# Kernel tuning notes

Hardware: AMD Instinct MI355X
Metric: run time of the kernel (lower is better)

Reference implementation:

```python
import jax, jax.numpy as jnp
import numpy as np

C = 256
NH = 8
G = 32  # groupnorm groups (min(32, C))
EPS = 1e-6


def setup_inputs() -> dict:
    key = jax.random.key(0)
    ks = jax.random.split(key, 7)
    B, D, H, W = 2, 16, 16, 16
    x = jax.random.normal(ks[0], (B, C, D, H, W), dtype=jnp.float32)
    gn_gamma = jnp.ones((C,), jnp.float32)
    gn_beta = jnp.zeros((C,), jnp.float32)
    s = 1.0 / np.sqrt(C)
    qkv_w = jax.random.normal(ks[1], (3 * C, C), jnp.float32) * s  # 1x1x1 conv weight
    qkv_b = jnp.zeros((3 * C,), jnp.float32)
    proj_w = jax.random.normal(ks[2], (C, C), jnp.float32) * s
    proj_b = jnp.zeros((C,), jnp.float32)
    return {"x": x, "gn_gamma": gn_gamma, "gn_beta": gn_beta,
            "qkv_w": qkv_w, "qkv_b": qkv_b, "proj_w": proj_w, "proj_b": proj_b}


def _group_norm(x, gamma, beta):
    # x: [B, C, S]
    B, Cc, S = x.shape
    xg = x.reshape(B, G, (Cc // G) * S)
    mu = xg.mean(axis=-1, keepdims=True)
    var = xg.var(axis=-1, keepdims=True)
    xg = (xg - mu) * jax.lax.rsqrt(var + EPS)
    x = xg.reshape(B, Cc, S)
    return x * gamma[None, :, None] + beta[None, :, None]


def reference(x, gn_gamma, gn_beta, qkv_w, qkv_b, proj_w, proj_b):
    B, Cc, D, H, W = x.shape
    S = D * H * W
    hd = Cc // NH
    xf = x.reshape(B, Cc, S)
    h = _group_norm(xf, gn_gamma, gn_beta)
    # 1x1x1 conv == channel matmul: [B, 3C, S]
    qkv = jnp.einsum('oc,bcs->bos', qkv_w, h) + qkv_b[None, :, None]
    # torch path: reshape(B,3C,S).permute(0,2,1).chunk -> q=channels[0:C]
    q, k, v = qkv[:, :Cc], qkv[:, Cc:2 * Cc], qkv[:, 2 * Cc:]
    # [B, C, S] -> [B, NH, S, hd]
    def to_heads(t):
        return t.reshape(B, NH, hd, S).transpose(0, 1, 3, 2)
    q, k, v = to_heads(q), to_heads(k), to_heads(v)
    scale = hd ** (-0.5)
    attn = jax.nn.softmax(jnp.einsum('bnqd,bnkd->bnqk', q, k) * scale, axis=-1)
    o = jnp.einsum('bnqk,bnkd->bnqd', attn, v)  # [B, NH, S, hd]
    o = o.transpose(0, 1, 3, 2).reshape(B, Cc, S)  # back to [B, C, S]
    o = jnp.einsum('oc,bcs->bos', proj_w, o) + proj_b[None, :, None]
    return x + o.reshape(B, Cc, D, H, W)
```

## Files before the change

kernel.cpp:

```cpp
#include <hip/hip_runtime.h>
#include <cstddef>

#define S_LEN 4096
#define C_DIM 256
#define NHEADS 8
#define HDIM 32

typedef __attribute__((ext_vector_type(8))) _Float16 half8;
typedef __attribute__((ext_vector_type(4))) _Float16 half4;
typedef __attribute__((ext_vector_type(2))) _Float16 h2t;
typedef __attribute__((ext_vector_type(2))) __fp16 fp16x2;
typedef __attribute__((ext_vector_type(4))) float floatx4;

#define SC2F ((float)(0.17677669529663687 * 1.4426950408889634))

__global__ __launch_bounds__(256) void prep_stats(
    const float* __restrict__ qkv_w, const float* __restrict__ proj_w,
    const float* __restrict__ qkv_b, const float* __restrict__ x,
    _Float16* __restrict__ wq, _Float16* __restrict__ wp,
    float* __restrict__ qbias, float* __restrict__ pstat)
{
  const int blk = blockIdx.x;
  const int tid = threadIdx.x;
  if (blk < 512) {
    __shared__ float red[2][4];
    const int gb = blk >> 3, e = blk & 7;
    const int g = gb & 31, b = gb >> 5;
    const float* xb = x + ((size_t)b * C_DIM + g * 8) * S_LEN + e * 4096;
    const float4* x4 = (const float4*)xb;
    float sum = 0.f, sumsq = 0.f;
    #pragma unroll
    for (int i = 0; i < 4; ++i) {
      float4 v = x4[tid + i * 256];
      sum += v.x + v.y + v.z + v.w;
      sumsq += v.x * v.x + v.y * v.y + v.z * v.z + v.w * v.w;
    }
    for (int off = 1; off < 64; off <<= 1) {
      sum += __shfl_xor(sum, off, 64);
      sumsq += __shfl_xor(sumsq, off, 64);
    }
    const int wv = tid >> 6, lane = tid & 63;
    if (lane == 0) { red[0][wv] = sum; red[1][wv] = sumsq; }
    __syncthreads();
    if (tid == 0) {
      pstat[(gb * 8 + e) * 2 + 0] = red[0][0] + red[0][1] + red[0][2] + red[0][3];
      pstat[(gb * 8 + e) * 2 + 1] = red[1][0] + red[1][1] + red[1][2] + red[1][3];
    }
  } else if (blk < 704) {
    const int i = (blk - 512) * 1024 + tid * 4;
    float4 v = *(const float4*)(qkv_w + i);
    const float sc = (i < 65536) ? SC2F : 1.f;
    half4 h = { (_Float16)(v.x * sc), (_Float16)(v.y * sc),
                (_Float16)(v.z * sc), (_Float16)(v.w * sc) };
    *(half4*)(wq + i) = h;
  } else if (blk < 768) {
    const int i = (blk - 704) * 1024 + tid * 4;
    float4 v = *(const float4*)(proj_w + i);
    half4 h = { (_Float16)v.x, (_Float16)v.y, (_Float16)v.z, (_Float16)v.w };
    *(half4*)(wp + i) = h;
  } else {
    #pragma unroll
    for (int j = 0; j < 3; ++j) {
      const int i = tid + j * 256;
      float bv = qkv_b[i];
      if (i < 256) bv *= SC2F;
      qbias[i] = bv;
    }
  }
}

__global__ __launch_bounds__(512) void qkv_gn_gemm(
    const _Float16* __restrict__ W, const float* __restrict__ bias,
    const float* __restrict__ x, const float* __restrict__ gamma,
    const float* __restrict__ beta, const float* __restrict__ pstat,
    _Float16* __restrict__ qo, _Float16* __restrict__ ko_,
    _Float16* __restrict__ vo)
{
  __shared__ __align__(16) _Float16 Ld[256 * 40];
  const int tid = threadIdx.x;
  const int b = blockIdx.y;
  const int s0 = blockIdx.x * 32;

  {
    const int c0 = (tid & 127) * 2, c1 = c0 + 1;
    const int sh = tid >> 7;
    const int gb = b * 32 + (c0 >> 3);
    float s = 0.f, sq = 0.f;
    #pragma unroll
    for (int e = 0; e < 8; ++e) {
      s  += pstat[(gb * 8 + e) * 2 + 0];
      sq += pstat[(gb * 8 + e) * 2 + 1];
    }
    const float mean = s * (1.f / 32768.f);
    const float rstd = rsqrtf(sq * (1.f / 32768.f) - mean * mean + 1e-6f);
    const float ga0 = gamma[c0] * rstd, be0 = beta[c0] - mean * ga0;
    const float ga1 = gamma[c1] * rstd, be1 = beta[c1] - mean * ga1;
    const float4* xa = (const float4*)(x + ((size_t)b * C_DIM + c0) * S_LEN + s0 + sh * 8);
    const float4* xc = (const float4*)(x + ((size_t)b * C_DIM + c1) * S_LEN + s0 + sh * 8);
    #pragma unroll
    for (int j = 0; j < 2; ++j) {
      float4 a = xa[j], c = xc[j];
      int sl = sh * 8 + j * 4;
      *(h2t*)&Ld[(sl + 0) * 264 + c0] = (h2t){ (_Float16)(a.x * ga0 + be0), (_Float16)(c.x * ga1 + be1) };
      *(h2t*)&Ld[(sl + 1) * 264 + c0] = (h2t){ (_Float16)(a.y * ga0 + be0), (_Float16)(c.y * ga1 + be1) };
      *(h2t*)&Ld[(sl + 2) * 264 + c0] = (h2t){ (_Float16)(a.z * ga0 + be0), (_Float16)(c.z * ga1 + be1) };
      *(h2t*)&Ld[(sl + 3) * 264 + c0] = (h2t){ (_Float16)(a.w * ga0 + be0), (_Float16)(c.w * ga1 + be1) };
    }
  }
  __syncthreads();

  const int lane = tid & 63, wv = tid >> 6;
  const int m = lane & 15, quad = lane >> 4;
  const _Float16* wrow[6];
  #pragma unroll
  for (int j = 0; j < 6; ++j)
    wrow[j] = W + (size_t)((wv + 8 * j) * 16 + m) * C_DIM + quad * 8;
  const _Float16* lp = &Ld[m * 264 + quad * 8];

  floatx4 acc[6][2];
  #pragma unroll
  for (int j = 0; j < 6; ++j) {
    acc[j][0] = (floatx4){0.f,0.f,0.f,0.f};
    acc[j][1] = (floatx4){0.f,0.f,0.f,0.f};
  }

  #pragma unroll 2
  for (int k0 = 0; k0 < C_DIM; k0 += 32) {
    half8 b0 = *(const half8*)(lp + k0);
    half8 b1 = *(const half8*)(lp + 16 * 264 + k0);
    #pragma unroll
    for (int j = 0; j < 6; ++j) {
      half8 a = *(const half8*)(wrow[j] + k0);
      acc[j][0] = __builtin_amdgcn_mfma_f32_16x16x32_f16(a, b0, acc[j][0], 0, 0, 0);
      acc[j][1] = __builtin_amdgcn_mfma_f32_16x16x32_f16(a, b1, acc[j][1], 0, 0, 0);
    }
  }

  __syncthreads();
  #pragma unroll
  for (int j = 0; j < 4; ++j) {
    const int ob = (wv + 8 * j) * 16 + quad * 4;
    const float bv0 = bias[ob], bv1 = bias[ob + 1],
                bv2 = bias[ob + 2], bv3 = bias[ob + 3];
    _Float16* dst = (ob < 256) ? qo : ko_;
    const int oo = ob & 255, n = oo >> 5, d0 = oo & 31;
    #pragma unroll
    for (int sub = 0; sub < 2; ++sub) {
      int s = s0 + sub * 16 + m;
      half4 h = { (_Float16)(acc[j][sub][0] + bv0), (_Float16)(acc[j][sub][1] + bv1),
                  (_Float16)(acc[j][sub][2] + bv2), (_Float16)(acc[j][sub][3] + bv3) };
      *(half4*)(dst + (((size_t)b * NHEADS + n) * S_LEN + s) * HDIM + d0) = h;
    }
  }
  _Float16* VLd = Ld;
  #pragma unroll
  for (int j = 4; j < 6; ++j) {
    const int ob = (wv + 8 * j) * 16 + quad * 4;
    const int lch = ob - 512;
    const float bv0 = bias[ob], bv1 = bias[ob + 1],
                bv2 = bias[ob + 2], bv3 = bias[ob + 3];
    #pragma unroll
    for (int sub = 0; sub < 2; ++sub) {
      int s = sub * 16 + m;
      VLd[(lch + 0) * 40 + s] = (_Float16)(acc[j][sub][0] + bv0);
      VLd[(lch + 1) * 40 + s] = (_Float16)(acc[j][sub][1] + bv1);
      VLd[(lch + 2) * 40 + s] = (_Float16)(acc[j][sub][2] + bv2);
      VLd[(lch + 3) * 40 + s] = (_Float16)(acc[j][sub][3] + bv3);
    }
  }
  __syncthreads();
  {
    const int ch = tid >> 1, sh = tid & 1;
    const int n = ch >> 5, d = ch & 31;
    _Float16* dst = vo + ((size_t)(b * NHEADS + n) * HDIM + d) * S_LEN + s0 + sh * 16;
    const _Float16* src = VLd + ch * 40 + sh * 16;
    *(half8*)(dst + 0) = *(const half8*)(src + 0);
    *(half8*)(dst + 8) = *(const half8*)(src + 8);
  }
}

__global__ __launch_bounds__(512) void attn_kernel(
    const _Float16* __restrict__ q, const _Float16* __restrict__ k,
    const _Float16* __restrict__ v, _Float16* __restrict__ o)
{
  __shared__ __align__(16) _Float16 Kl[2][128 * 40];
  __shared__ __align__(16) _Float16 Vl[2][32 * 136];
  const int tid = threadIdx.x;
  const int lane = tid & 63, wv = tid >> 6;
  const int m = lane & 15, quad = lane >> 4;
  const int n = blockIdx.y, b = blockIdx.z;
  const int qc = blockIdx.x;
  const int q0 = qc * 256 + wv * 32;
  const int bh = b * NHEADS + n;

  const _Float16* qb = q + (size_t)bh * S_LEN * HDIM;
  const _Float16* kb = k + (size_t)bh * S_LEN * HDIM;
  const _Float16* vb = v + (size_t)bh * HDIM * S_LEN;

  half8 qfA = *(const half8*)(qb + (size_t)(q0 + m) * HDIM + quad * 8);
  half8 qfB = *(const half8*)(qb + (size_t)(q0 + 16 + m) * HDIM + quad * 8);

  const int krow = wv * 16 + (lane >> 2), kc = (lane & 3) * 8;
  const int vrow = wv * 4 + (lane >> 4), vc = (lane & 15) * 8;
  const _Float16* kg = kb + (size_t)krow * HDIM + kc;
  const _Float16* vg = vb + (size_t)vrow * S_LEN + vc;
  const int klds = krow * 40 + kc;
  const int vlds = vrow * 136 + vc;

  int4 kreg = *(const int4*)kg;
  int4 vreg = *(const int4*)vg;
  const _Float16* kgp = kg + 128 * HDIM;
  const _Float16* vgp = vg + 128;

  floatx4 oA0 = {0.f,0.f,0.f,0.f}, oA1 = oA0, oB0 = oA0, oB1 = oA0;
  float lA0 = 0.f, lA1 = 0.f, lB0 = 0.f, lB1 = 0.f;
  const fp16x2 one2 = { (__fp16)1.0f, (__fp16)1.0f };
  const floatx4 zz = {0.f,0.f,0.f,0.f};

  #pragma unroll 2
  for (int it = 0; it < 32; ++it) {
    const int bufi = it & 1;
    *(int4*)(&Kl[bufi][klds]) = kreg;
    *(int4*)(&Vl[bufi][vlds]) = vreg;
    kreg = *(const int4*)kgp; kgp += 128 * HDIM;
    vreg = *(const int4*)vgp; vgp += 128;
    __syncthreads();
    const _Float16* Kb = Kl[bufi];
    const _Float16* Vb = Vl[bufi];

    #pragma unroll
    for (int t = 0; t < 8; ++t) {
      const int tt = (t + wv) & 7;
      half8 kf  = *(const half8*)(Kb + (tt * 16 + m) * 40 + quad * 8);
      half4 vf0 = *(const half4*)(Vb + m * 136 + tt * 16 + quad * 4);
      half4 vf1 = *(const half4*)(Vb + (16 + m) * 136 + tt * 16 + quad * 4);
      __builtin_amdgcn_s_setprio(1);
      floatx4 sA = __builtin_amdgcn_mfma_f32_16x16x32_f16(kf, qfA, zz, 0, 0, 0);
      floatx4 sB = __builtin_amdgcn_mfma_f32_16x16x32_f16(kf, qfB, zz, 0, 0, 0);
      __builtin_amdgcn_s_setprio(0);
      float eA0 = __builtin_amdgcn_exp2f(sA[0]);
      float eA1 = __builtin_amdgcn_exp2f(sA[1]);
      float eA2 = __builtin_amdgcn_exp2f(sA[2]);
      float eA3 = __builtin_amdgcn_exp2f(sA[3]);
      float eB0 = __builtin_amdgcn_exp2f(sB[0]);
      float eB1 = __builtin_amdgcn_exp2f(sB[1]);
      float eB2 = __builtin_amdgcn_exp2f(sB[2]);
      float eB3 = __builtin_amdgcn_exp2f(sB[3]);
      half4 pA, pB;
      fp16x2 pAlo = __builtin_amdgcn_cvt_pkrtz(eA0, eA1);
      fp16x2 pAhi = __builtin_amdgcn_cvt_pkrtz(eA2, eA3);
      fp16x2 pBlo = __builtin_amdgcn_cvt_pkrtz(eB0, eB1);
      fp16x2 pBhi = __builtin_amdgcn_cvt_pkrtz(eB2, eB3);
      *(fp16x2*)&pA = pAlo; *((fp16x2*)&pA + 1) = pAhi;
      *(fp16x2*)&pB = pBlo; *((fp16x2*)&pB + 1) = pBhi;
      lA0 = __builtin_amdgcn_fdot2(pAlo, one2, lA0, false);
      lA1 = __builtin_amdgcn_fdot2(pAhi, one2, lA1, false);
      lB0 = __builtin_amdgcn_fdot2(pBlo, one2, lB0, false);
      lB1 = __builtin_amdgcn_fdot2(pBhi, one2, lB1, false);
      __builtin_amdgcn_s_setprio(1);
      oA0 = __builtin_amdgcn_mfma_f32_16x16x16f16(vf0, pA, oA0, 0, 0, 0);
      oA1 = __builtin_amdgcn_mfma_f32_16x16x16f16(vf1, pA, oA1, 0, 0, 0);
      oB0 = __builtin_amdgcn_mfma_f32_16x16x16f16(vf0, pB, oB0, 0, 0, 0);
      oB1 = __builtin_amdgcn_mfma_f32_16x16x16f16(vf1, pB, oB1, 0, 0, 0);
      __builtin_amdgcn_s_setprio(0);
    }
  }
  float lA = lA0 + lA1, lB = lB0 + lB1;
  lA += __shfl_xor(lA, 16, 64); lA += __shfl_xor(lA, 32, 64);
  lB += __shfl_xor(lB, 16, 64); lB += __shfl_xor(lB, 32, 64);
  const float rA = 1.f / lA, rB = 1.f / lB;
  _Float16* obase = o + ((size_t)bh * S_LEN) * HDIM;
  {
    _Float16* oh = obase + (size_t)(q0 + m) * HDIM;
    half4 h0 = { (_Float16)(oA0[0] * rA), (_Float16)(oA0[1] * rA),
                 (_Float16)(oA0[2] * rA), (_Float16)(oA0[3] * rA) };
    half4 h1 = { (_Float16)(oA1[0] * rA), (_Float16)(oA1[1] * rA),
                 (_Float16)(oA1[2] * rA), (_Float16)(oA1[3] * rA) };
    *(half4*)(oh + quad * 4) = h0;
    *(half4*)(oh + 16 + quad * 4) = h1;
  }
  {
    _Float16* oh = obase + (size_t)(q0 + 16 + m) * HDIM;
    half4 h0 = { (_Float16)(oB0[0] * rB), (_Float16)(oB0[1] * rB),
                 (_Float16)(oB0[2] * rB), (_Float16)(oB0[3] * rB) };
    half4 h1 = { (_Float16)(oB1[0] * rB), (_Float16)(oB1[1] * rB),
                 (_Float16)(oB1[2] * rB), (_Float16)(oB1[3] * rB) };
    *(half4*)(oh + quad * 4) = h0;
    *(half4*)(oh + 16 + quad * 4) = h1;
  }
}

__global__ __launch_bounds__(256) void proj_gemm(
    const _Float16* __restrict__ W, const float* __restrict__ bias,
    const _Float16* __restrict__ o,
    const float* __restrict__ x, float* __restrict__ out)
{
  const int tid = threadIdx.x;
  const int lane = tid & 63, wv = tid >> 6;
  const int m = lane & 15, quad = lane >> 4;
  const int mtb = blockIdx.x * 8 + wv * 2;
  const int s0 = blockIdx.y * 64;
  const int b = blockIdx.z;

  const _Float16* wrow0 = W + (size_t)((mtb + 0) * 16 + m) * C_DIM + quad * 8;
  const _Float16* wrow1 = W + (size_t)((mtb + 1) * 16 + m) * C_DIM + quad * 8;
  floatx4 acc[2][4];
  #pragma unroll
  for (int j = 0; j < 2; ++j)
    #pragma unroll
    for (int s = 0; s < 4; ++s) acc[j][s] = (floatx4){0.f,0.f,0.f,0.f};

  #pragma unroll
  for (int k0 = 0; k0 < C_DIM; k0 += 32) {
    const int n = k0 >> 5;
    const int d0 = quad * 8;
    half8 bf[4];
    #pragma unroll
    for (int sub = 0; sub < 4; ++sub) {
      size_t idx = (((size_t)(b * NHEADS + n)) * S_LEN + s0 + sub * 16 + m) * HDIM + d0;
      bf[sub] = *(const half8*)(o + idx);
    }
    half8 af0 = *(const half8*)(wrow0 + k0);
    half8 af1 = *(const half8*)(wrow1 + k0);
    #pragma unroll
    for (int sub = 0; sub < 4; ++sub) {
      acc[0][sub] = __builtin_amdgcn_mfma_f32_16x16x32_f16(af0, bf[sub], acc[0][sub], 0, 0, 0);
      acc[1][sub] = __builtin_amdgcn_mfma_f32_16x16x32_f16(af1, bf[sub], acc[1][sub], 0, 0, 0);
    }
  }
  #pragma unroll
  for (int j = 0; j < 2; ++j)
    #pragma unroll
    for (int sub = 0; sub < 4; ++sub) {
      int s = s0 + sub * 16 + m;
      #pragma unroll
      for (int r = 0; r < 4; ++r) {
        int c = (mtb + j) * 16 + quad * 4 + r;
        size_t idx = ((size_t)b * C_DIM + c) * S_LEN + s;
        out[idx] = x[idx] + acc[j][sub][r] + bias[c];
      }
    }
}

extern "C" void kernel_launch(void* const* d_in, const int* in_sizes, int n_in,
                              void* d_out, int out_size, void* d_ws, size_t ws_size,
                              hipStream_t stream) {
  const float* x        = (const float*)d_in[0];
  const float* gn_gamma = (const float*)d_in[1];
  const float* gn_beta  = (const float*)d_in[2];
  const float* qkv_w    = (const float*)d_in[3];
  const float* qkv_b    = (const float*)d_in[4];
  const float* proj_w   = (const float*)d_in[5];
  const float* proj_b   = (const float*)d_in[6];
  float* out = (float*)d_out;

  const size_t n1 = (size_t)2 * S_LEN * C_DIM;
  char* ws = (char*)d_ws;
  _Float16* qx  = (_Float16*)ws;
  _Float16* kx  = qx + n1;
  _Float16* vx  = kx + n1;
  _Float16* wq  = vx + n1;
  _Float16* wp  = wq + 768 * 256;
  float*    qbias = (float*)(wp + 256 * 256);
  float*    pstat = qbias + 768;
  _Float16* ox  = (_Float16*)(pstat + 1024);

  prep_stats<<<769, 256, 0, stream>>>(qkv_w, proj_w, qkv_b, x, wq, wp, qbias, pstat);
  qkv_gn_gemm<<<dim3(128, 2), 512, 0, stream>>>(wq, qbias, x, gn_gamma, gn_beta, pstat, qx, kx, vx);
  attn_kernel<<<dim3(16, 8, 2), 512, 0, stream>>>(qx, kx, vx, ox);
  proj_gemm<<<dim3(2, 64, 2), 256, 0, stream>>>(wp, proj_b, ox, x, out);
}
```

Before: 144.6 us.

## Fuse attention with output projection, loading K/V directly from global memory

Merges the attention and projection kernels into one. Each block handles 32 query positions across all 8 heads (one wave per head), stages the normalized output in LDS, and then runs the projection GEMM plus residual add in place. The LDS double-buffered K/V staging is replaced by direct global (L2-cached) register loads, software-pipelined in groups of four. This removes the intermediate output round-trip and a kernel launch. The cost is that each wave streams the full K/V for its head with no block-level sharing, so L2 traffic rises a lot and each block does less work on the attention side.

```diff
diff --git a/kernel.cpp b/kernel.cpp
--- a/kernel.cpp
+++ b/kernel.cpp
@@ -179,165 +179,140 @@
   }
 }
 
-__global__ __launch_bounds__(512) void attn_kernel(
+#define LOADG(KF, V0, V1, G) do {                                         \
+    const int _g4 = (G) * 4;                                              \
+    _Pragma("unroll")                                                     \
+    for (int _t = 0; _t < 4; ++_t) {                                      \
+      KF[_t] = *(const half8*)(kaddr + (size_t)(_g4 + _t) * 512);         \
+      V0[_t] = *(const half4*)(vaddr0 + (_g4 + _t) * 16);                 \
+      V1[_t] = *(const half4*)(vaddr1 + (_g4 + _t) * 16);                 \
+    }                                                                     \
+  } while (0)
+
+#define COMPG(KF, V0, V1) do {                                            \
+    _Pragma("unroll")                                                     \
+    for (int _t = 0; _t < 4; ++_t) {                                      \
+      __builtin_amdgcn_s_setprio(1);                                      \
+      floatx4 sA = __builtin_amdgcn_mfma_f32_16x16x32_f16(KF[_t], qfA, zz, 0, 0, 0); \
+      floatx4 sB = __builtin_amdgcn_mfma_f32_16x16x32_f16(KF[_t], qfB, zz, 0, 0, 0); \
+      __builtin_amdgcn_s_setprio(0);                                      \
+      float eA0 = __builtin_amdgcn_exp2f(sA[0]);                          \
+      float eA1 = __builtin_amdgcn_exp2f(sA[1]);                          \
+      float eA2 = __builtin_amdgcn_exp2f(sA[2]);                          \
+      float eA3 = __builtin_amdgcn_exp2f(sA[3]);                          \
+      float eB0 = __builtin_amdgcn_exp2f(sB[0]);                          \
+      float eB1 = __builtin_amdgcn_exp2f(sB[1]);                          \
+      float eB2 = __builtin_amdgcn_exp2f(sB[2]);                          \
+      float eB3 = __builtin_amdgcn_exp2f(sB[3]);                          \
+      half4 pA, pB;                                                       \
+      fp16x2 pAlo = __builtin_amdgcn_cvt_pkrtz(eA0, eA1);                 \
+      fp16x2 pAhi = __builtin_amdgcn_cvt_pkrtz(eA2, eA3);                 \
+      fp16x2 pBlo = __builtin_amdgcn_cvt_pkrtz(eB0, eB1);                 \
+      fp16x2 pBhi = __builtin_amdgcn_cvt_pkrtz(eB2, eB3);                 \
+      *(fp16x2*)&pA = pAlo; *((fp16x2*)&pA + 1) = pAhi;                   \
+      *(fp16x2*)&pB = pBlo; *((fp16x2*)&pB + 1) = pBhi;                   \
+      lA0 = __builtin_amdgcn_fdot2(pAlo, one2, lA0, false);               \
+      lA1 = __builtin_amdgcn_fdot2(pAhi, one2, lA1, false);               \
+      lB0 = __builtin_amdgcn_fdot2(pBlo, one2, lB0, false);               \
+      lB1 = __builtin_amdgcn_fdot2(pBhi, one2, lB1, false);               \
+      __builtin_amdgcn_s_setprio(1);                                      \
+      oA0 = __builtin_amdgcn_mfma_f32_16x16x16f16(V0[_t], pA, oA0, 0, 0, 0); \
+      oA1 = __builtin_amdgcn_mfma_f32_16x16x16f16(V1[_t], pA, oA1, 0, 0, 0); \
+      oB0 = __builtin_amdgcn_mfma_f32_16x16x16f16(V0[_t], pB, oB0, 0, 0, 0); \
+      oB1 = __builtin_amdgcn_mfma_f32_16x16x16f16(V1[_t], pB, oB1, 0, 0, 0); \
+      __builtin_amdgcn_s_setprio(0);                                      \
+    }                                                                     \
+  } while (0)
+
+__global__ __launch_bounds__(512, 2) void attn_proj(
     const _Float16* __restrict__ q, const _Float16* __restrict__ k,
-    const _Float16* __restrict__ v, _Float16* __restrict__ o)
+    const _Float16* __restrict__ v, const _Float16* __restrict__ wp,
+    const float* __restrict__ pbias, const float* __restrict__ x,
+    float* __restrict__ out)
 {
-  __shared__ __align__(16) _Float16 Kl[2][128 * 40];
-  __shared__ __align__(16) _Float16 Vl[2][32 * 136];
+  __shared__ __align__(16) _Float16 Lo[32 * 264];
   const int tid = threadIdx.x;
   const int lane = tid & 63, wv = tid >> 6;
   const int m = lane & 15, quad = lane >> 4;
-  const int n = blockIdx.y, b = blockIdx.z;
-  const int qc = blockIdx.x;
-  const int q0 = qc * 256 + wv * 32;
-  const int bh = b * NHEADS + n;
+  const int b = blockIdx.y;
+  const int sbase = blockIdx.x * 32;
+  const int bh = b * NHEADS + wv;
 
   const _Float16* qb = q + (size_t)bh * S_LEN * HDIM;
-  const _Float16* kb = k + (size_t)bh * S_LEN * HDIM;
+  const _Float16* kaddr = k + (size_t)bh * S_LEN * HDIM + m * HDIM + quad * 8;
   const _Float16* vb = v + (size_t)bh * HDIM * S_LEN;
-
-  half8 qfA = *(const half8*)(qb + (size_t)(q0 + m) * HDIM + quad * 8);
-  half8 qfB = *(const half8*)(qb + (size_t)(q0 + 16 + m) * HDIM + quad * 8);
-
-  const int krow = wv * 16 + (lane >> 2), kc = (lane & 3) * 8;
-  const int vrow = wv * 4 + (lane >> 4), vc = (lane & 15) * 8;
-  const _Float16* kg = kb + (size_t)krow * HDIM + kc;
-  const _Float16* vg = vb + (size_t)vrow * S_LEN + vc;
-  const int klds = krow * 40 + kc;
-  const int vlds = vrow * 136 + vc;
-
-  int4 kreg = *(const int4*)kg;
-  int4 vreg = *(const int4*)vg;
-  const _Float16* kgp = kg + 128 * HDIM;
-  const _Float16* vgp = vg + 128;
+  const _Float16* vaddr0 = vb + (size_t)m * S_LEN + quad * 4;
+  const _Float16* vaddr1 = vb + (size_t)(16 + m) * S_LEN + quad * 4;
+
+  half8 qfA = *(const half8*)(qb + (size_t)(sbase + m) * HDIM + quad * 8);
+  half8 qfB = *(const half8*)(qb + (size_t)(sbase + 16 + m) * HDIM + quad * 8);
 
   floatx4 oA0 = {0.f,0.f,0.f,0.f}, oA1 = oA0, oB0 = oA0, oB1 = oA0;
   float lA0 = 0.f, lA1 = 0.f, lB0 = 0.f, lB1 = 0.f;
   const fp16x2 one2 = { (__fp16)1.0f, (__fp16)1.0f };
   const floatx4 zz = {0.f,0.f,0.f,0.f};
 
-  #pragma unroll 2
-  for (int it = 0; it < 32; ++it) {
-    const int bufi = it & 1;
-    *(int4*)(&Kl[bufi][klds]) = kreg;
-    *(int4*)(&Vl[bufi][vlds]) = vreg;
-    kreg = *(const int4*)kgp; kgp += 128 * HDIM;
-    vreg = *(const int4*)vgp; vgp += 128;
-    __syncthreads();
-    const _Float16* Kb = Kl[bufi];
-    const _Float16* Vb = Vl[bufi];
-
-    #pragma unroll
-    for (int t = 0; t < 8; ++t) {
-      const int tt = (t + wv) & 7;
-      half8 kf  = *(const half8*)(Kb + (tt * 16 + m) * 40 + quad * 8);
-      half4 vf0 = *(const half4*)(Vb + m * 136 + tt * 16 + quad * 4);
-      half4 vf1 = *(const half4*)(Vb + (16 + m) * 136 + tt * 16 + quad * 4);
-      __builtin_amdgcn_s_setprio(1);
-      floatx4 sA = __builtin_amdgcn_mfma_f32_16x16x32_f16(kf, qfA, zz, 0, 0, 0);
-      floatx4 sB = __builtin_amdgcn_mfma_f32_16x16x32_f16(kf, qfB, zz, 0, 0, 0);
-      __builtin_amdgcn_s_setprio(0);
-      float eA0 = __builtin_amdgcn_exp2f(sA[0]);
-      float eA1 = __builtin_amdgcn_exp2f(sA[1]);
-      float eA2 = __builtin_amdgcn_exp2f(sA[2]);
-      float eA3 = __builtin_amdgcn_exp2f(sA[3]);
-      float eB0 = __builtin_amdgcn_exp2f(sB[0]);
-      float eB1 = __builtin_amdgcn_exp2f(sB[1]);
-      float eB2 = __builtin_amdgcn_exp2f(sB[2]);
-      float eB3 = __builtin_amdgcn_exp2f(sB[3]);
-      half4 pA, pB;
-      fp16x2 pAlo = __builtin_amdgcn_cvt_pkrtz(eA0, eA1);
-      fp16x2 pAhi = __builtin_amdgcn_cvt_pkrtz(eA2, eA3);
-      fp16x2 pBlo = __builtin_amdgcn_cvt_pkrtz(eB0, eB1);
-      fp16x2 pBhi = __builtin_amdgcn_cvt_pkrtz(eB2, eB3);
-      *(fp16x2*)&pA = pAlo; *((fp16x2*)&pA + 1) = pAhi;
-      *(fp16x2*)&pB = pBlo; *((fp16x2*)&pB + 1) = pBhi;
-      lA0 = __builtin_amdgcn_fdot2(pAlo, one2, lA0, false);
-      lA1 = __builtin_amdgcn_fdot2(pAhi, one2, lA1, false);
-      lB0 = __builtin_amdgcn_fdot2(pBlo, one2, lB0, false);
-      lB1 = __builtin_amdgcn_fdot2(pBhi, one2, lB1, false);
-      __builtin_amdgcn_s_setprio(1);
-      oA0 = __builtin_amdgcn_mfma_f32_16x16x16f16(vf0, pA, oA0, 0, 0, 0);
-      oA1 = __builtin_amdgcn_mfma_f32_16x16x16f16(vf1, pA, oA1, 0, 0, 0);
-      oB0 = __builtin_amdgcn_mfma_f32_16x16x16f16(vf0, pB, oB0, 0, 0, 0);
-      oB1 = __builtin_amdgcn_mfma_f32_16x16x16f16(vf1, pB, oB1, 0, 0, 0);
-      __builtin_amdgcn_s_setprio(0);
-    }
-  }
+  half8 kfA[4], kfB[4];
+  half4 v0A[4], v1A[4], v0B[4], v1B[4];
+
+  LOADG(kfA, v0A, v1A, 0);
+  for (int g = 0; g < 64; g += 2) {
+    LOADG(kfB, v0B, v1B, g + 1);
+    COMPG(kfA, v0A, v1A);
+    if (g + 2 < 64) LOADG(kfA, v0A, v1A, g + 2);
+    COMPG(kfB, v0B, v1B);
+  }
+
   float lA = lA0 + lA1, lB = lB0 + lB1;
   lA += __shfl_xor(lA, 16, 64); lA += __shfl_xor(lA, 32, 64);
   lB += __shfl_xor(lB, 16, 64); lB += __shfl_xor(lB, 32, 64);
   const float rA = 1.f / lA, rB = 1.f / lB;
-  _Float16* obase = o + ((size_t)bh * S_LEN) * HDIM;
+
   {
-    _Float16* oh = obase + (size_t)(q0 + m) * HDIM;
-    half4 h0 = { (_Float16)(oA0[0] * rA), (_Float16)(oA0[1] * rA),
-                 (_Float16)(oA0[2] * rA), (_Float16)(oA0[3] * rA) };
-    half4 h1 = { (_Float16)(oA1[0] * rA), (_Float16)(oA1[1] * rA),
-                 (_Float16)(oA1[2] * rA), (_Float16)(oA1[3] * rA) };
-    *(half4*)(oh + quad * 4) = h0;
-    *(half4*)(oh + 16 + quad * 4) = h1;
-  }
-  {
-    _Float16* oh = obase + (size_t)(q0 + 16 + m) * HDIM;
-    half4 h0 = { (_Float16)(oB0[0] * rB), (_Float16)(oB0[1] * rB),
-                 (_Float16)(oB0[2] * rB), (_Float16)(oB0[3] * rB) };
-    half4 h1 = { (_Float16)(oB1[0] * rB), (_Float16)(oB1[1] * rB),
-                 (_Float16)(oB1[2] * rB), (_Float16)(oB1[3] * rB) };
-    *(half4*)(oh + quad * 4) = h0;
-    *(half4*)(oh + 16 + quad * 4) = h1;
-  }
-}
-
-__global__ __launch_bounds__(256) void proj_gemm(
-    const _Float16* __restrict__ W, const float* __restrict__ bias,
-    const _Float16* __restrict__ o,
-    const float* __restrict__ x, float* __restrict__ out)
-{
-  const int tid = threadIdx.x;
-  const int lane = tid & 63, wv = tid >> 6;
-  const int m = lane & 15, quad = lane >> 4;
-  const int mtb = blockIdx.x * 8 + wv * 2;
-  const int s0 = blockIdx.y * 64;
-  const int b = blockIdx.z;
-
-  const _Float16* wrow0 = W + (size_t)((mtb + 0) * 16 + m) * C_DIM + quad * 8;
-  const _Float16* wrow1 = W + (size_t)((mtb + 1) * 16 + m) * C_DIM + quad * 8;
-  floatx4 acc[2][4];
-  #pragma unroll
-  for (int j = 0; j < 2; ++j)
-    #pragma unroll
-    for (int s = 0; s < 4; ++s) acc[j][s] = (floatx4){0.f,0.f,0.f,0.f};
+    const int chA = wv * 32 + quad * 4;
+    half4 hA0 = { (_Float16)(oA0[0] * rA), (_Float16)(oA0[1] * rA),
+                  (_Float16)(oA0[2] * rA), (_Float16)(oA0[3] * rA) };
+    half4 hA1 = { (_Float16)(oA1[0] * rA), (_Float16)(oA1[1] * rA),
+                  (_Float16)(oA1[2] * rA), (_Float16)(oA1[3] * rA) };
+    half4 hB0 = { (_Float16)(oB0[0] * rB), (_Float16)(oB0[1] * rB),
+                  (_Float16)(oB0[2] * rB), (_Float16)(oB0[3] * rB) };
+    half4 hB1 = { (_Float16)(oB1[0] * rB), (_Float16)(oB1[1] * rB),
+                  (_Float16)(oB1[2] * rB), (_Float16)(oB1[3] * rB) };
+    *(half4*)&Lo[m * 264 + chA]            = hA0;
+    *(half4*)&Lo[m * 264 + chA + 16]       = hA1;
+    *(half4*)&Lo[(16 + m) * 264 + chA]     = hB0;
+    *(half4*)&Lo[(16 + m) * 264 + chA + 16]= hB1;
+  }
+  __syncthreads();
+
+  const int mtb = wv * 2;
+  const _Float16* wrow0 = wp + (size_t)((mtb + 0) * 16 + m) * C_DIM + quad * 8;
+  const _Float16* wrow1 = wp + (size_t)((mtb + 1) * 16 + m) * C_DIM + quad * 8;
+  floatx4 acc[2][2];
+  acc[0][0] = (floatx4){0.f,0.f,0.f,0.f}; acc[0][1] = acc[0][0];
+  acc[1][0] = acc[0][0]; acc[1][1] = acc[0][0];
 
   #pragma unroll
   for (int k0 = 0; k0 < C_DIM; k0 += 32) {
-    const int n = k0 >> 5;
-    const int d0 = quad * 8;
-    half8 bf[4];
-    #pragma unroll
-    for (int sub = 0; sub < 4; ++sub) {
-      size_t idx = (((size_t)(b * NHEADS + n)) * S_LEN + s0 + sub * 16 + m) * HDIM + d0;
-      bf[sub] = *(const half8*)(o + idx);
-    }
+    half8 bf0 = *(const half8*)&Lo[m * 264 + k0 + quad * 8];
+    half8 bf1 = *(const half8*)&Lo[(16 + m) * 264 + k0 + quad * 8];
     half8 af0 = *(const half8*)(wrow0 + k0);
     half8 af1 = *(const half8*)(wrow1 + k0);
-    #pragma unroll
-    for (int sub = 0; sub < 4; ++sub) {
-      acc[0][sub] = __builtin_amdgcn_mfma_f32_16x16x32_f16(af0, bf[sub], acc[0][sub], 0, 0, 0);
-      acc[1][sub] = __builtin_amdgcn_mfma_f32_16x16x32_f16(af1, bf[sub], acc[1][sub], 0, 0, 0);
-    }
+    acc[0][0] = __builtin_amdgcn_mfma_f32_16x16x32_f16(af0, bf0, acc[0][0], 0, 0, 0);
+    acc[0][1] = __builtin_amdgcn_mfma_f32_16x16x32_f16(af0, bf1, acc[0][1], 0, 0, 0);
+    acc[1][0] = __builtin_amdgcn_mfma_f32_16x16x32_f16(af1, bf0, acc[1][0], 0, 0, 0);
+    acc[1][1] = __builtin_amdgcn_mfma_f32_16x16x32_f16(af1, bf1, acc[1][1], 0, 0, 0);
   }
   #pragma unroll
   for (int j = 0; j < 2; ++j)
     #pragma unroll
-    for (int sub = 0; sub < 4; ++sub) {
-      int s = s0 + sub * 16 + m;
+    for (int sub = 0; sub < 2; ++sub) {
+      int s = sbase + sub * 16 + m;
       #pragma unroll
       for (int r = 0; r < 4; ++r) {
         int c = (mtb + j) * 16 + quad * 4 + r;
         size_t idx = ((size_t)b * C_DIM + c) * S_LEN + s;
-        out[idx] = x[idx] + acc[j][sub][r] + bias[c];
+        out[idx] = x[idx] + acc[j][sub][r] + pbias[c];
       }
     }
 }
@@ -363,10 +338,8 @@
   _Float16* wp  = wq + 768 * 256;
   float*    qbias = (float*)(wp + 256 * 256);
   float*    pstat = qbias + 768;
-  _Float16* ox  = (_Float16*)(pstat + 1024);
 
   prep_stats<<<769, 256, 0, stream>>>(qkv_w, proj_w, qkv_b, x, wq, wp, qbias, pstat);
   qkv_gn_gemm<<<dim3(128, 2), 512, 0, stream>>>(wq, qbias, x, gn_gamma, gn_beta, pstat, qx, kx, vx);
-  attn_kernel<<<dim3(16, 8, 2), 512, 0, stream>>>(qx, kx, vx, ox);
-  proj_gemm<<<dim3(2, 64, 2), 256, 0, stream>>>(wp, proj_b, ox, x, out);
+  attn_proj<<<dim3(128, 2), 512, 0, stream>>>(qx, kx, vx, wp, proj_b, x, out);
 }
```

Result: slower. 236.5 us (+63.6%).

## Switch attention inner loop to 32x32x16 MFMA with permlane32 swap for P

Applied to the files above, without the earlier changes.

Rewrites the attention inner loop to use 32x32x16 f16 MFMAs for both QK^T and PV, with one 32-query tile per wave, instead of pairs of 16x16 MFMAs. The exponentiated scores are packed to fp16 and rearranged across half-waves with v_permlane32_swap, so the S accumulator layout becomes the B operand layout without going through LDS. The K LDS row padding changes from 40 to 36 elements, and launch bounds request two blocks per CU. The intent is fewer MFMA issues with larger tiles and fewer LDS fragment loads, at the cost of a 16-wide accumulator per wave and more register pressure.

```diff
diff --git a/kernel.cpp b/kernel.cpp
--- a/kernel.cpp
+++ b/kernel.cpp
@@ -11,6 +11,7 @@
 typedef __attribute__((ext_vector_type(2))) _Float16 h2t;
 typedef __attribute__((ext_vector_type(2))) __fp16 fp16x2;
 typedef __attribute__((ext_vector_type(4))) float floatx4;
+typedef __attribute__((ext_vector_type(16))) float floatx16;
 
 #define SC2F ((float)(0.17677669529663687 * 1.4426950408889634))
 
@@ -179,15 +180,15 @@
   }
 }
 
-__global__ __launch_bounds__(512) void attn_kernel(
+__global__ __launch_bounds__(512, 2) void attn_kernel(
     const _Float16* __restrict__ q, const _Float16* __restrict__ k,
     const _Float16* __restrict__ v, _Float16* __restrict__ o)
 {
-  __shared__ __align__(16) _Float16 Kl[2][128 * 40];
+  __shared__ __align__(16) _Float16 Kl[2][128 * 36];
   __shared__ __align__(16) _Float16 Vl[2][32 * 136];
   const int tid = threadIdx.x;
   const int lane = tid & 63, wv = tid >> 6;
-  const int m = lane & 15, quad = lane >> 4;
+  const int l31 = lane & 31, hi = lane >> 5;
   const int n = blockIdx.y, b = blockIdx.z;
   const int qc = blockIdx.x;
   const int q0 = qc * 256 + wv * 32;
@@ -197,14 +198,14 @@
   const _Float16* kb = k + (size_t)bh * S_LEN * HDIM;
   const _Float16* vb = v + (size_t)bh * HDIM * S_LEN;
 
-  half8 qfA = *(const half8*)(qb + (size_t)(q0 + m) * HDIM + quad * 8);
-  half8 qfB = *(const half8*)(qb + (size_t)(q0 + 16 + m) * HDIM + quad * 8);
+  half8 qf1 = *(const half8*)(qb + (size_t)(q0 + l31) * HDIM + hi * 8);
+  half8 qf2 = *(const half8*)(qb + (size_t)(q0 + l31) * HDIM + 16 + hi * 8);
 
   const int krow = wv * 16 + (lane >> 2), kc = (lane & 3) * 8;
   const int vrow = wv * 4 + (lane >> 4), vc = (lane & 15) * 8;
   const _Float16* kg = kb + (size_t)krow * HDIM + kc;
   const _Float16* vg = vb + (size_t)vrow * S_LEN + vc;
-  const int klds = krow * 40 + kc;
+  const int klds = krow * 36 + kc;
   const int vlds = vrow * 136 + vc;
 
   int4 kreg = *(const int4*)kg;
@@ -212,10 +213,11 @@
   const _Float16* kgp = kg + 128 * HDIM;
   const _Float16* vgp = vg + 128;
 
-  floatx4 oA0 = {0.f,0.f,0.f,0.f}, oA1 = oA0, oB0 = oA0, oB1 = oA0;
-  float lA0 = 0.f, lA1 = 0.f, lB0 = 0.f, lB1 = 0.f;
+  floatx16 oacc;
+  #pragma unroll
+  for (int i = 0; i < 16; ++i) oacc[i] = 0.f;
+  float l0 = 0.f, l1 = 0.f;
   const fp16x2 one2 = { (__fp16)1.0f, (__fp16)1.0f };
-  const floatx4 zz = {0.f,0.f,0.f,0.f};
 
   #pragma unroll 2
   for (int it = 0; it < 32; ++it) {
@@ -229,64 +231,62 @@
     const _Float16* Vb = Vl[bufi];
 
     #pragma unroll
-    for (int t = 0; t < 8; ++t) {
-      const int tt = (t + wv) & 7;
-      half8 kf  = *(const half8*)(Kb + (tt * 16 + m) * 40 + quad * 8);
-      half4 vf0 = *(const half4*)(Vb + m * 136 + tt * 16 + quad * 4);
-      half4 vf1 = *(const half4*)(Vb + (16 + m) * 136 + tt * 16 + quad * 4);
+    for (int t = 0; t < 4; ++t) {
+      const int tt = (t + wv) & 3;
+      const int k32 = tt * 32;
+      half8 kf1 = *(const half8*)(Kb + (k32 + l31) * 36 + hi * 8);
+      half8 kf2 = *(const half8*)(Kb + (k32 + l31) * 36 + 16 + hi * 8);
+      half8 vf1 = *(const half8*)(Vb + l31 * 136 + k32 + hi * 8);
+      half8 vf2 = *(const half8*)(Vb + l31 * 136 + k32 + 16 + hi * 8);
+
+      floatx16 sD;
+      #pragma unroll
+      for (int i = 0; i < 16; ++i) sD[i] = 0.f;
       __builtin_amdgcn_s_setprio(1);
-      floatx4 sA = __builtin_amdgcn_mfma_f32_16x16x32_f16(kf, qfA, zz, 0, 0, 0);
-      floatx4 sB = __builtin_amdgcn_mfma_f32_16x16x32_f16(kf, qfB, zz, 0, 0, 0);
+      sD = __builtin_amdgcn_mfma_f32_32x32x16_f16(kf1, qf1, sD, 0, 0, 0);
+      sD = __builtin_amdgcn_mfma_f32_32x32x16_f16(kf2, qf2, sD, 0, 0, 0);
       __builtin_amdgcn_s_setprio(0);
-      float eA0 = __builtin_amdgcn_exp2f(sA[0]);
-      float eA1 = __builtin_amdgcn_exp2f(sA[1]);
-      float eA2 = __builtin_amdgcn_exp2f(sA[2]);
-      float eA3 = __builtin_amdgcn_exp2f(sA[3]);
-      float eB0 = __builtin_amdgcn_exp2f(sB[0]);
-      float eB1 = __builtin_amdgcn_exp2f(sB[1]);
-      float eB2 = __builtin_amdgcn_exp2f(sB[2]);
-      float eB3 = __builtin_amdgcn_exp2f(sB[3]);
-      half4 pA, pB;
-      fp16x2 pAlo = __builtin_amdgcn_cvt_pkrtz(eA0, eA1);
-      fp16x2 pAhi = __builtin_amdgcn_cvt_pkrtz(eA2, eA3);
-      fp16x2 pBlo = __builtin_amdgcn_cvt_pkrtz(eB0, eB1);
-      fp16x2 pBhi = __builtin_amdgcn_cvt_pkrtz(eB2, eB3);
-      *(fp16x2*)&pA = pAlo; *((fp16x2*)&pA + 1) = pAhi;
-      *(fp16x2*)&pB = pBlo; *((fp16x2*)&pB + 1) = pBhi;
-      lA0 = __builtin_amdgcn_fdot2(pAlo, one2, lA0, false);
-      lA1 = __builtin_amdgcn_fdot2(pAhi, one2, lA1, false);
-      lB0 = __builtin_amdgcn_fdot2(pBlo, one2, lB0, false);
-      lB1 = __builtin_amdgcn_fdot2(pBhi, one2, lB1, false);
+
+      int g[8];
+      #pragma unroll
+      for (int i = 0; i < 8; ++i) {
+        float e0 = __builtin_amdgcn_exp2f(sD[2 * i]);
+        float e1 = __builtin_amdgcn_exp2f(sD[2 * i + 1]);
+        fp16x2 p = __builtin_amdgcn_cvt_pkrtz(e0, e1);
+        g[i] = __builtin_bit_cast(int, p);
+      }
+      l0 = __builtin_amdgcn_fdot2(__builtin_bit_cast(fp16x2, g[0]), one2, l0, false);
+      l0 = __builtin_amdgcn_fdot2(__builtin_bit_cast(fp16x2, g[1]), one2, l0, false);
+      l0 = __builtin_amdgcn_fdot2(__builtin_bit_cast(fp16x2, g[2]), one2, l0, false);
+      l0 = __builtin_amdgcn_fdot2(__builtin_bit_cast(fp16x2, g[3]), one2, l0, false);
+      l1 = __builtin_amdgcn_fdot2(__builtin_bit_cast(fp16x2, g[4]), one2, l1, false);
+      l1 = __builtin_amdgcn_fdot2(__builtin_bit_cast(fp16x2, g[5]), one2, l1, false);
+      l1 = __builtin_amdgcn_fdot2(__builtin_bit_cast(fp16x2, g[6]), one2, l1, false);
+      l1 = __builtin_amdgcn_fdot2(__builtin_bit_cast(fp16x2, g[7]), one2, l1, false);
+
+      asm volatile("v_permlane32_swap_b32 %0, %1" : "+v"(g[0]), "+v"(g[2]));
+      asm volatile("v_permlane32_swap_b32 %0, %1" : "+v"(g[1]), "+v"(g[3]));
+      asm volatile("v_permlane32_swap_b32 %0, %1" : "+v"(g[4]), "+v"(g[6]));
+      asm volatile("v_permlane32_swap_b32 %0, %1" : "+v"(g[5]), "+v"(g[7]));
+      union { half8 h; int u[4]; } B1, B2;
+      B1.u[0] = g[0]; B1.u[1] = g[1]; B1.u[2] = g[2]; B1.u[3] = g[3];
+      B2.u[0] = g[4]; B2.u[1] = g[5]; B2.u[2] = g[6]; B2.u[3] = g[7];
+
       __builtin_amdgcn_s_setprio(1);
-      oA0 = __builtin_amdgcn_mfma_f32_16x16x16f16(vf0, pA, oA0, 0, 0, 0);
-      oA1 = __builtin_amdgcn_mfma_f32_16x16x16f16(vf1, pA, oA1, 0, 0, 0);
-      oB0 = __builtin_amdgcn_mfma_f32_16x16x16f16(vf0, pB, oB0, 0, 0, 0);
-      oB1 = __builtin_amdgcn_mfma_f32_16x16x16f16(vf1, pB, oB1, 0, 0, 0);
+      oacc = __builtin_amdgcn_mfma_f32_32x32x16_f16(vf1, B1.h, oacc, 0, 0, 0);
+      oacc = __builtin_amdgcn_mfma_f32_32x32x16_f16(vf2, B2.h, oacc, 0, 0, 0);
       __builtin_amdgcn_s_setprio(0);
     }
   }
-  float lA = lA0 + lA1, lB = lB0 + lB1;
-  lA += __shfl_xor(lA, 16, 64); lA += __shfl_xor(lA, 32, 64);
-  lB += __shfl_xor(lB, 16, 64); lB += __shfl_xor(lB, 32, 64);
-  const float rA = 1.f / lA, rB = 1.f / lB;
-  _Float16* obase = o + ((size_t)bh * S_LEN) * HDIM;
-  {
-    _Float16* oh = obase + (size_t)(q0 + m) * HDIM;
-    half4 h0 = { (_Float16)(oA0[0] * rA), (_Float16)(oA0[1] * rA),
-                 (_Float16)(oA0[2] * rA), (_Float16)(oA0[3] * rA) };
-    half4 h1 = { (_Float16)(oA1[0] * rA), (_Float16)(oA1[1] * rA),
-                 (_Float16)(oA1[2] * rA), (_Float16)(oA1[3] * rA) };
-    *(half4*)(oh + quad * 4) = h0;
-    *(half4*)(oh + 16 + quad * 4) = h1;
-  }
-  {
-    _Float16* oh = obase + (size_t)(q0 + 16 + m) * HDIM;
-    half4 h0 = { (_Float16)(oB0[0] * rB), (_Float16)(oB0[1] * rB),
-                 (_Float16)(oB0[2] * rB), (_Float16)(oB0[3] * rB) };
-    half4 h1 = { (_Float16)(oB1[0] * rB), (_Float16)(oB1[1] * rB),
-                 (_Float16)(oB1[2] * rB), (_Float16)(oB1[3] * rB) };
-    *(half4*)(oh + quad * 4) = h0;
-    *(half4*)(oh + 16 + quad * 4) = h1;
+  float l = l0 + l1;
+  l += __shfl_xor(l, 32, 64);
+  const float r = 1.f / l;
+  _Float16* oh = o + ((size_t)bh * S_LEN + q0 + l31) * HDIM + hi * 4;
+  #pragma unroll
+  for (int t2 = 0; t2 < 4; ++t2) {
+    half4 h = { (_Float16)(oacc[4 * t2 + 0] * r), (_Float16)(oacc[4 * t2 + 1] * r),
+                (_Float16)(oacc[4 * t2 + 2] * r), (_Float16)(oacc[4 * t2 + 3] * r) };
+    *(half4*)(oh + 8 * t2) = h;
   }
 }
 
```

After: 168.4 us. 1.16x slower.
